# Kernel optimization log

Hardware: AMD Instinct MI355X
Metric: run time of the kernel (lower is better)

The kernel has to match this reference:

```python
import jax, jax.numpy as jnp
import numpy as np

N = 100000      # nodes
E = 1600000     # nonzeros in sparse H (avg degree 16)
IN_DIM = 128
HID = 128
OUT = 128


def setup_inputs() -> dict:
    key = jax.random.key(0)
    k = jax.random.split(key, 8)
    X = jax.random.normal(k[0], (N, IN_DIM), dtype=jnp.float32)
    H_rows = jax.random.randint(k[1], (E,), 0, N, dtype=jnp.int32)
    H_cols = jax.random.randint(k[2], (E,), 0, N, dtype=jnp.int32)
    H_vals = jax.random.uniform(k[3], (E,), dtype=jnp.float32)
    # Linear params (PyTorch: y = x @ W.T + b); store as [in, out] for x @ W
    s1 = 1.0 / np.sqrt(IN_DIM)
    s2 = 1.0 / np.sqrt(HID)
    W1 = jax.random.uniform(k[4], (IN_DIM, HID), jnp.float32, -s1, s1)
    b1 = jax.random.uniform(k[5], (HID,), jnp.float32, -s1, s1)
    W2 = jax.random.uniform(k[6], (HID, OUT), jnp.float32, -s2, s2)
    b2 = jax.random.uniform(k[7], (OUT,), jnp.float32, -s2, s2)
    return {"X": X, "H_rows": H_rows, "H_cols": H_cols, "H_vals": H_vals,
            "W1": W1, "b1": b1, "W2": W2, "b2": b2}


def _spmm(rows, cols, vals, X):
    # sparse [N,N] @ dense [N,d] via edge gather + segment-sum
    msgs = vals[:, None] * X[cols]            # [E, d]
    return jax.ops.segment_sum(msgs, rows, num_segments=N)


def reference(X, H_rows, H_cols, H_vals, W1, b1, W2, b2):
    # num_layers == 2 branch; dropout is identity (eval mode)
    h = _spmm(H_rows, H_cols, H_vals, X @ W1 + b1)   # H @ W1(X)
    h = jax.nn.relu(h)
    out = _spmm(H_rows, H_cols, H_vals, h @ W2 + b2) # H @ W2(h)
    return out
```

## Files before the change

### kernel.cpp

```cpp
#include <hip/hip_runtime.h>

#define NNODES 100000
#define DIM 128
#define BROWS 256
#define NB ((NNODES + BROWS - 1) / BROWS)
#define BCAP 5120
#define CHUNK 4096

typedef _Float16 half8 __attribute__((ext_vector_type(8)));
typedef float f32x4 __attribute__((ext_vector_type(4)));
typedef unsigned int u32x4 __attribute__((ext_vector_type(4)));
typedef unsigned long long u64;

__device__ __forceinline__ unsigned int pack_bf16x2(float lo, float hi) {
    unsigned int ul = __float_as_uint(lo);
    unsigned int uh = __float_as_uint(hi);
    ul = (ul + 0x7fffu + ((ul >> 16) & 1u)) >> 16;
    uh = (uh + 0x7fffu + ((uh >> 16) & 1u)) & 0xffff0000u;
    return uh | ul;
}

__device__ __forceinline__ void unpack_bf16x8_v(u32x4 v, float* f) {
    f[0] = __uint_as_float(v.x << 16); f[1] = __uint_as_float(v.x & 0xffff0000u);
    f[2] = __uint_as_float(v.y << 16); f[3] = __uint_as_float(v.y & 0xffff0000u);
    f[4] = __uint_as_float(v.z << 16); f[5] = __uint_as_float(v.z & 0xffff0000u);
    f[6] = __uint_as_float(v.w << 16); f[7] = __uint_as_float(v.w & 0xffff0000u);
}

template <bool IN_BF16>
__device__ __forceinline__ void gemm_body(int blk, const void* __restrict__ Ain,
                                          const _Float16* __restrict__ Wt,
                                          const float* __restrict__ bias,
                                          unsigned short* __restrict__ Yb, int n) {
    const int t = threadIdx.x;
    const int l = t & 63;
    const int lr = l & 15;
    const int lg = l >> 4;
    const int r0 = blk * 128 + (t >> 6) * 32;

    half8 xf[2][4];
#pragma unroll
    for (int rt = 0; rt < 2; ++rt) {
        const int row = r0 + rt * 16 + lr;
        const bool ok = row < n;
        if (IN_BF16) {
            const u32x4* __restrict__ A16 = (const u32x4*)Ain;
#pragma unroll
            for (int ks = 0; ks < 4; ++ks) {
                u32x4 v = {0u, 0u, 0u, 0u};
                if (ok) v = __builtin_nontemporal_load(&A16[(size_t)row * 16 + ks * 4 + lg]);
                float f[8];
                unpack_bf16x8_v(v, f);
                half8 h;
#pragma unroll
                for (int j = 0; j < 8; ++j) h[j] = (_Float16)f[j];
                xf[rt][ks] = h;
            }
        } else {
            const f32x4* __restrict__ A4 = (const f32x4*)Ain;
#pragma unroll
            for (int ks = 0; ks < 4; ++ks) {
                f32x4 v0 = {0.f, 0.f, 0.f, 0.f};
                f32x4 v1 = v0;
                if (ok) {
                    v0 = __builtin_nontemporal_load(&A4[(size_t)row * 32 + ks * 8 + lg * 2]);
                    v1 = __builtin_nontemporal_load(&A4[(size_t)row * 32 + ks * 8 + lg * 2 + 1]);
                }
                half8 h;
                h[0] = (_Float16)v0.x; h[1] = (_Float16)v0.y;
                h[2] = (_Float16)v0.z; h[3] = (_Float16)v0.w;
                h[4] = (_Float16)v1.x; h[5] = (_Float16)v1.y;
                h[6] = (_Float16)v1.z; h[7] = (_Float16)v1.w;
                xf[rt][ks] = h;
            }
        }
    }

    const f32x4 zero4 = {0.f, 0.f, 0.f, 0.f};
    f32x4 acc[2][8];
#pragma unroll
    for (int rt = 0; rt < 2; ++rt)
#pragma unroll
        for (int ct = 0; ct < 8; ++ct) acc[rt][ct] = zero4;

    const half8* __restrict__ Wf = (const half8*)Wt;
#pragma unroll
    for (int ct = 0; ct < 8; ++ct) {
        half8 wf[4];
#pragma unroll
        for (int ks = 0; ks < 4; ++ks)
            wf[ks] = Wf[(ct * 16 + lr) * 16 + ks * 4 + lg];
#pragma unroll
        for (int ks = 0; ks < 4; ++ks) {
            acc[0][ct] = __builtin_amdgcn_mfma_f32_16x16x32_f16(wf[ks], xf[0][ks], acc[0][ct], 0, 0, 0);
            acc[1][ct] = __builtin_amdgcn_mfma_f32_16x16x32_f16(wf[ks], xf[1][ks], acc[1][ct], 0, 0, 0);
        }
    }

#pragma unroll
    for (int ct = 0; ct < 8; ++ct) {
        const int c0 = ct * 16 + lg * 4;
        const float4 bv = *(const float4*)&bias[c0];
#pragma unroll
        for (int rt = 0; rt < 2; ++rt) {
            const int row = r0 + rt * 16 + lr;
            if (row < n) {
                f32x4 a = acc[rt][ct];
                const uint2 pv = make_uint2(pack_bf16x2(a[0] + bv.x, a[1] + bv.y),
                                            pack_bf16x2(a[2] + bv.z, a[3] + bv.w));
                *(uint2*)&Yb[(size_t)row * DIM + c0] = pv;
            }
        }
    }
}

__global__ __launch_bounds__(256) void gemm_mfma_bf16(const void* __restrict__ Ain,
                                                      const _Float16* __restrict__ Wt,
                                                      const float* __restrict__ bias,
                                                      unsigned short* __restrict__ Yb, int n) {
    gemm_body<true>(blockIdx.x, Ain, Wt, bias, Yb, n);
}

__global__ __launch_bounds__(256) void pass1_bin(const int* __restrict__ rows,
                                                 const int* __restrict__ cols,
                                                 const float* __restrict__ vals,
                                                 int* __restrict__ bcnt,
                                                 int2* __restrict__ tmp, int nnz,
                                                 int p1_blocks,
                                                 const float* __restrict__ W1s,
                                                 const float* __restrict__ W2s,
                                                 _Float16* __restrict__ Wt1,
                                                 _Float16* __restrict__ Wt2) {
    __shared__ int hist[NB];
    __shared__ int base[NB];
    __shared__ int cur[NB];
    const int t = threadIdx.x;

    if (blockIdx.x >= (unsigned)p1_blocks) {
        const int b = blockIdx.x - p1_blocks;
        const float* __restrict__ W = (b & 4) ? W2s : W1s;
        _Float16* __restrict__ Wt = (b & 4) ? Wt2 : Wt1;
        const int base2 = (b & 3) * 4096;
        for (int i = t; i < 4096; i += 256) {
            const int e = base2 + i;
            const int k = e >> 7, c = e & 127;
            Wt[c * 128 + k] = (_Float16)W[e];
        }
        return;
    }

    const int e0 = blockIdx.x * CHUNK;
    const int e1 = min(e0 + CHUNK, nnz);

    for (int i = t; i < NB; i += 256) { hist[i] = 0; cur[i] = 0; }
    __syncthreads();

    for (int i = e0 + t; i < e1; i += 256)
        atomicAdd(&hist[rows[i] >> 8], 1);
    __syncthreads();

    for (int i = t; i < NB; i += 256)
        base[i] = (hist[i] > 0) ? atomicAdd(&bcnt[i], hist[i]) : 0;
    __syncthreads();

    for (int i = e0 + t; i < e1; i += 256) {
        const int r = rows[i];
        const int b = r >> 8;
        const int pos = base[b] + atomicAdd(&cur[b], 1);
        if (pos < BCAP)
            tmp[(size_t)b * BCAP + pos] =
                make_int2(((r & 255) << 24) | cols[i], __float_as_int(vals[i]));
    }
}

__global__ __launch_bounds__(256) void pass2_gemm1(const int2* __restrict__ tmp,
                                                   const int* __restrict__ bcnt,
                                                   int2* __restrict__ epack,
                                                   int* __restrict__ row_ptr,
                                                   int* __restrict__ counts,
                                                   const float* __restrict__ X,
                                                   const _Float16* __restrict__ Wt1,
                                                   const float* __restrict__ b1,
                                                   unsigned short* __restrict__ Yb, int n) {
    __shared__ int cnt[256];
    __shared__ int s[256];
    __shared__ int cur[256];

    if (blockIdx.x >= NB) {
        gemm_body<false>(blockIdx.x - NB, X, Wt1, b1, Yb, n);
        return;
    }

    const int b = blockIdx.x;
    const int t = threadIdx.x;
    const int row0 = b * BROWS;
    const int nrows = min(BROWS, n - row0);
    const int m = min(bcnt[b], BCAP);
    const int2* __restrict__ src = tmp + (size_t)b * BCAP;

    int partial = 0;
    for (int i = t; i < b; i += 256) partial += bcnt[i];
    s[t] = partial;
    __syncthreads();
    for (int off = 128; off >= 1; off >>= 1) {
        if (t < off) s[t] += s[t + off];
        __syncthreads();
    }
    const int base = s[0];
    __syncthreads();

    cnt[t] = 0;
    __syncthreads();
    for (int i = t; i < m; i += 256)
        atomicAdd(&cnt[((unsigned)src[i].x) >> 24], 1);
    __syncthreads();

    const int v = cnt[t];
    s[t] = v;
    __syncthreads();
    for (int off = 1; off < 256; off <<= 1) {
        int x = (t >= off) ? s[t - off] : 0;
        __syncthreads();
        s[t] += x;
        __syncthreads();
    }
    const int excl = s[t] - v;
    if (t < nrows) {
        row_ptr[row0 + t] = base + excl;
        counts[row0 + t] = v;
    }
    cur[t] = base + excl;
    __syncthreads();

    for (int i = t; i < m; i += 256) {
        const int2 e = src[i];
        const int rl = ((unsigned)e.x) >> 24;
        const int pos = atomicAdd(&cur[rl], 1);
        epack[pos] = make_int2(e.x & 0xFFFFFF, e.y);
    }
}

template <bool RELU_OUT, bool OUT_BF16>
__global__ __launch_bounds__(256) void spmm_csr(const int* __restrict__ row_ptr,
                                                const int* __restrict__ counts,
                                                const int2* __restrict__ epack,
                                                const unsigned short* __restrict__ Xb,
                                                void* __restrict__ out, int n) {
    const int gid = blockIdx.x * blockDim.x + threadIdx.x;
    const int r = gid >> 4;
    const int lane = gid & 15;
    if (r >= n) return;
    const int start = row_ptr[r];
    const int cnt = counts[r];
    const u32x4* __restrict__ X16 = (const u32x4*)Xb;
    const u64* __restrict__ ep = (const u64*)(epack + start);

    float acc[8];
#pragma unroll
    for (int k = 0; k < 8; ++k) acc[k] = 0.f;

    int j = 0;
    for (; j + 4 <= cnt; j += 4) {
        const u64 e0 = __builtin_nontemporal_load(&ep[j]);
        const u64 e1 = __builtin_nontemporal_load(&ep[j + 1]);
        const u64 e2 = __builtin_nontemporal_load(&ep[j + 2]);
        const u64 e3 = __builtin_nontemporal_load(&ep[j + 3]);
        const u32x4 x0 = X16[(size_t)(unsigned)(e0 & 0xffffffffu) * 16 + lane];
        const u32x4 x1 = X16[(size_t)(unsigned)(e1 & 0xffffffffu) * 16 + lane];
        const u32x4 x2 = X16[(size_t)(unsigned)(e2 & 0xffffffffu) * 16 + lane];
        const u32x4 x3 = X16[(size_t)(unsigned)(e3 & 0xffffffffu) * 16 + lane];
        const float v0 = __uint_as_float((unsigned)(e0 >> 32));
        const float v1 = __uint_as_float((unsigned)(e1 >> 32));
        const float v2 = __uint_as_float((unsigned)(e2 >> 32));
        const float v3 = __uint_as_float((unsigned)(e3 >> 32));
        float f0[8], f1[8], f2[8], f3[8];
        unpack_bf16x8_v(x0, f0); unpack_bf16x8_v(x1, f1);
        unpack_bf16x8_v(x2, f2); unpack_bf16x8_v(x3, f3);
#pragma unroll
        for (int k = 0; k < 8; ++k)
            acc[k] += v0 * f0[k] + v1 * f1[k] + v2 * f2[k] + v3 * f3[k];
    }
    for (; j < cnt; ++j) {
        const u64 e = __builtin_nontemporal_load(&ep[j]);
        const u32x4 x = X16[(size_t)(unsigned)(e & 0xffffffffu) * 16 + lane];
        const float v = __uint_as_float((unsigned)(e >> 32));
        float f[8];
        unpack_bf16x8_v(x, f);
#pragma unroll
        for (int k = 0; k < 8; ++k) acc[k] += v * f[k];
    }

    if (RELU_OUT) {
#pragma unroll
        for (int k = 0; k < 8; ++k) acc[k] = fmaxf(acc[k], 0.f);
    }

    if (OUT_BF16) {
        u32x4 pv;
        pv.x = pack_bf16x2(acc[0], acc[1]); pv.y = pack_bf16x2(acc[2], acc[3]);
        pv.z = pack_bf16x2(acc[4], acc[5]); pv.w = pack_bf16x2(acc[6], acc[7]);
        __builtin_nontemporal_store(pv, (u32x4*)out + (size_t)r * 16 + lane);
    } else {
        float* of = (float*)out;
        f32x4 a0 = {acc[0], acc[1], acc[2], acc[3]};
        f32x4 a1 = {acc[4], acc[5], acc[6], acc[7]};
        __builtin_nontemporal_store(a0, (f32x4*)&of[(size_t)r * DIM + lane * 8]);
        __builtin_nontemporal_store(a1, (f32x4*)&of[(size_t)r * DIM + lane * 8 + 4]);
    }
}

extern "C" void kernel_launch(void* const* d_in, const int* in_sizes, int n_in,
                              void* d_out, int out_size, void* d_ws, size_t ws_size,
                              hipStream_t stream) {
    const float* X      = (const float*)d_in[0];
    const int*   H_rows = (const int*)d_in[1];
    const int*   H_cols = (const int*)d_in[2];
    const float* H_vals = (const float*)d_in[3];
    const float* W1     = (const float*)d_in[4];
    const float* b1     = (const float*)d_in[5];
    const float* W2     = (const float*)d_in[6];
    const float* b2     = (const float*)d_in[7];
    float* out = (float*)d_out;

    const int E = in_sizes[1];
    const int N = NNODES;
    const size_t bmat_bytes = (size_t)N * DIM * 2;

    const int gemm_blocks = (N + 127) / 128;
    const int p1_blocks = (E + CHUNK - 1) / CHUNK;
    const int spmm_blocks = (N * 16 + 255) / 256;

    char* p = (char*)d_ws;
    unsigned short* Yb = (unsigned short*)p;  p += bmat_bytes;
    unsigned short* hb = (unsigned short*)p;  p += bmat_bytes;
    _Float16* Wt1      = (_Float16*)p;        p += 128 * 128 * 2;
    _Float16* Wt2      = (_Float16*)p;        p += 128 * 128 * 2;
    int2* epack        = (int2*)p;            p += (size_t)E * 8;
    int2* tmp          = (int2*)p;            p += (size_t)NB * BCAP * 8;
    int*  bcnt         = (int*)p;             p += (size_t)NB * 4;
    int*  row_ptr      = (int*)p;             p += (size_t)N * 4;
    int*  counts       = (int*)p;             p += (size_t)N * 4;

    hipMemsetAsync(bcnt, 0, (size_t)NB * 4, stream);
    pass1_bin<<<p1_blocks + 8, 256, 0, stream>>>(H_rows, H_cols, H_vals, bcnt, tmp, E,
                                                 p1_blocks, W1, W2, Wt1, Wt2);

    pass2_gemm1<<<NB + gemm_blocks, 256, 0, stream>>>(tmp, bcnt, epack, row_ptr, counts,
                                                      X, Wt1, b1, Yb, N);

    spmm_csr<true, true><<<spmm_blocks, 256, 0, stream>>>(row_ptr, counts, epack, Yb, hb, N);

    gemm_mfma_bf16<<<gemm_blocks, 256, 0, stream>>>(hb, Wt2, b2, Yb, N);
    spmm_csr<false, false><<<spmm_blocks, 256, 0, stream>>>(row_ptr, counts, epack, Yb, out, N);
}
```

Measured before the change: 365.2 us.

## Slice SpMM feature dimension across blocks to shrink per-block gather footprint

The SpMM kernel now splits the 128-wide feature dimension into 8 slices of 16 features, handled by consecutive blocks. Each block covers 128 rows with 2 threads per row, so each 32-byte slice of X rows is gathered by many rows at once, aiming for better cache locality for the random column gathers. The GEMM input loads and the bf16 SpMM store drop their nontemporal hints so the data stays in cache for later kernels. The cost is that every slice block re-reads the same edge list (8x edge-index traffic) and the gathers become 32-byte segments, which are less efficient per transaction.

```diff
diff --git a/kernel.cpp b/kernel.cpp
--- a/kernel.cpp
+++ b/kernel.cpp
@@ -48,7 +48,7 @@
 #pragma unroll
             for (int ks = 0; ks < 4; ++ks) {
                 u32x4 v = {0u, 0u, 0u, 0u};
-                if (ok) v = __builtin_nontemporal_load(&A16[(size_t)row * 16 + ks * 4 + lg]);
+                if (ok) v = A16[(size_t)row * 16 + ks * 4 + lg];
                 float f[8];
                 unpack_bf16x8_v(v, f);
                 half8 h;
@@ -63,8 +63,8 @@
                 f32x4 v0 = {0.f, 0.f, 0.f, 0.f};
                 f32x4 v1 = v0;
                 if (ok) {
-                    v0 = __builtin_nontemporal_load(&A4[(size_t)row * 32 + ks * 8 + lg * 2]);
-                    v1 = __builtin_nontemporal_load(&A4[(size_t)row * 32 + ks * 8 + lg * 2 + 1]);
+                    v0 = A4[(size_t)row * 32 + ks * 8 + lg * 2];
+                    v1 = A4[(size_t)row * 32 + ks * 8 + lg * 2 + 1];
                 }
                 half8 h;
                 h[0] = (_Float16)v0.x; h[1] = (_Float16)v0.y;
@@ -241,19 +241,23 @@
 }
 
 template <bool RELU_OUT, bool OUT_BF16>
-__global__ __launch_bounds__(256) void spmm_csr(const int* __restrict__ row_ptr,
-                                                const int* __restrict__ counts,
-                                                const int2* __restrict__ epack,
-                                                const unsigned short* __restrict__ Xb,
-                                                void* __restrict__ out, int n) {
-    const int gid = blockIdx.x * blockDim.x + threadIdx.x;
-    const int r = gid >> 4;
-    const int lane = gid & 15;
+__global__ __launch_bounds__(256) void spmm_sliced(const int* __restrict__ row_ptr,
+                                                   const int* __restrict__ counts,
+                                                   const int2* __restrict__ epack,
+                                                   const unsigned short* __restrict__ Xb,
+                                                   void* __restrict__ out, int n) {
+    const int s = blockIdx.x & 7;
+    const int g = blockIdx.x >> 3;
+    const int t = threadIdx.x;
+    const int lane = t & 1;
+    const int r = g * 128 + (t >> 1);
     if (r >= n) return;
+
     const int start = row_ptr[r];
     const int cnt = counts[r];
     const u32x4* __restrict__ X16 = (const u32x4*)Xb;
     const u64* __restrict__ ep = (const u64*)(epack + start);
+    const int xoff = s * 2 + lane;
 
     float acc[8];
 #pragma unroll
@@ -265,10 +269,10 @@
         const u64 e1 = __builtin_nontemporal_load(&ep[j + 1]);
         const u64 e2 = __builtin_nontemporal_load(&ep[j + 2]);
         const u64 e3 = __builtin_nontemporal_load(&ep[j + 3]);
-        const u32x4 x0 = X16[(size_t)(unsigned)(e0 & 0xffffffffu) * 16 + lane];
-        const u32x4 x1 = X16[(size_t)(unsigned)(e1 & 0xffffffffu) * 16 + lane];
-        const u32x4 x2 = X16[(size_t)(unsigned)(e2 & 0xffffffffu) * 16 + lane];
-        const u32x4 x3 = X16[(size_t)(unsigned)(e3 & 0xffffffffu) * 16 + lane];
+        const u32x4 x0 = X16[(size_t)(unsigned)(e0 & 0xffffffffu) * 16 + xoff];
+        const u32x4 x1 = X16[(size_t)(unsigned)(e1 & 0xffffffffu) * 16 + xoff];
+        const u32x4 x2 = X16[(size_t)(unsigned)(e2 & 0xffffffffu) * 16 + xoff];
+        const u32x4 x3 = X16[(size_t)(unsigned)(e3 & 0xffffffffu) * 16 + xoff];
         const float v0 = __uint_as_float((unsigned)(e0 >> 32));
         const float v1 = __uint_as_float((unsigned)(e1 >> 32));
         const float v2 = __uint_as_float((unsigned)(e2 >> 32));
@@ -282,7 +286,7 @@
     }
     for (; j < cnt; ++j) {
         const u64 e = __builtin_nontemporal_load(&ep[j]);
-        const u32x4 x = X16[(size_t)(unsigned)(e & 0xffffffffu) * 16 + lane];
+        const u32x4 x = X16[(size_t)(unsigned)(e & 0xffffffffu) * 16 + xoff];
         const float v = __uint_as_float((unsigned)(e >> 32));
         float f[8];
         unpack_bf16x8_v(x, f);
@@ -299,13 +303,13 @@
         u32x4 pv;
         pv.x = pack_bf16x2(acc[0], acc[1]); pv.y = pack_bf16x2(acc[2], acc[3]);
         pv.z = pack_bf16x2(acc[4], acc[5]); pv.w = pack_bf16x2(acc[6], acc[7]);
-        __builtin_nontemporal_store(pv, (u32x4*)out + (size_t)r * 16 + lane);
+        ((u32x4*)out)[(size_t)r * 16 + xoff] = pv;
     } else {
         float* of = (float*)out;
         f32x4 a0 = {acc[0], acc[1], acc[2], acc[3]};
         f32x4 a1 = {acc[4], acc[5], acc[6], acc[7]};
-        __builtin_nontemporal_store(a0, (f32x4*)&of[(size_t)r * DIM + lane * 8]);
-        __builtin_nontemporal_store(a1, (f32x4*)&of[(size_t)r * DIM + lane * 8 + 4]);
+        __builtin_nontemporal_store(a0, (f32x4*)&of[(size_t)r * DIM + xoff * 8]);
+        __builtin_nontemporal_store(a1, (f32x4*)&of[(size_t)r * DIM + xoff * 8 + 4]);
     }
 }
 
@@ -328,7 +332,7 @@
 
     const int gemm_blocks = (N + 127) / 128;
     const int p1_blocks = (E + CHUNK - 1) / CHUNK;
-    const int spmm_blocks = (N * 16 + 255) / 256;
+    const int spmm_blocks = 8 * ((N + 127) / 128);
 
     char* p = (char*)d_ws;
     unsigned short* Yb = (unsigned short*)p;  p += bmat_bytes;
@@ -348,8 +352,8 @@
     pass2_gemm1<<<NB + gemm_blocks, 256, 0, stream>>>(tmp, bcnt, epack, row_ptr, counts,
                                                       X, Wt1, b1, Yb, N);
 
-    spmm_csr<true, true><<<spmm_blocks, 256, 0, stream>>>(row_ptr, counts, epack, Yb, hb, N);
+    spmm_sliced<true, true><<<spmm_blocks, 256, 0, stream>>>(row_ptr, counts, epack, Yb, hb, N);
 
     gemm_mfma_bf16<<<gemm_blocks, 256, 0, stream>>>(hb, Wt2, b2, Yb, N);
-    spmm_csr<false, false><<<spmm_blocks, 256, 0, stream>>>(row_ptr, counts, epack, Yb, out, N);
-}
+    spmm_sliced<false, false><<<spmm_blocks, 256, 0, stream>>>(row_ptr, counts, epack, Yb, out, N);
+}
```

Measured after the change: 710.4 us. 94.5% more time.
